# Kernel tuning notes

Hardware: AMD Instinct MI355X
Metric: run time of the kernel (lower is better)

## Reference

```python
import jax, jax.numpy as jnp
import numpy as np
import math

EMBED_SIZE = 2048
HEADS = 32
GROUPS = 8
HEAD_DIM = EMBED_SIZE // HEADS          # 64
HPG = HEADS // GROUPS                   # heads per group = 4
N, L = 4, 1024


def setup_inputs() -> dict:
    key = jax.random.key(0)
    k1, k2, k3, k4, k5 = jax.random.split(key, 5)
    values = jax.random.normal(k1, (N, L, EMBED_SIZE), dtype=jnp.float32)
    keys = jax.random.normal(k2, (N, L, EMBED_SIZE), dtype=jnp.float32)
    queries = jax.random.normal(k3, (N, L, EMBED_SIZE), dtype=jnp.float32)
    mask = jnp.ones((N, 1, 1, L, L), dtype=jnp.int32)
    # fc_out: Linear(heads*head_dim -> embed_size), torch default init ~ U(-1/sqrt(in), 1/sqrt(in))
    bound = 1.0 / math.sqrt(EMBED_SIZE)
    W_out = jax.random.uniform(k4, (EMBED_SIZE, EMBED_SIZE), jnp.float32, -bound, bound)
    b_out = jax.random.uniform(k5, (EMBED_SIZE,), jnp.float32, -bound, bound)
    return {"values": values, "keys": keys, "queries": queries, "mask": mask,
            "W_out": W_out, "b_out": b_out}


def reference(values, keys, queries, mask, W_out, b_out):
    n, q_len, _ = queries.shape
    k_len = keys.shape[1]
    # split into (N, L, groups, heads_per_group, head_dim)
    v = values.reshape(n, k_len, GROUPS, HPG, HEAD_DIM)
    k = keys.reshape(n, k_len, GROUPS, HPG, HEAD_DIM)
    q = queries.reshape(n, q_len, GROUPS, HPG, HEAD_DIM)
    # scores: (N, groups, heads_per_group, q, k)
    energy = jnp.einsum('nqghd,nkghd->nghqk', q, k)
    energy = jnp.where(mask == 0, jnp.float32(-1e20), energy)
    attn = jax.nn.softmax(energy / jnp.sqrt(jnp.float32(EMBED_SIZE)), axis=-1)
    out = jnp.einsum('nghqk,nkghd->nqghd', attn, v).reshape(n, q_len, EMBED_SIZE)
    return out @ W_out.T + b_out
```

## Files before the change

kernel.cpp:

```cpp
#include <hip/hip_runtime.h>
#include <math.h>


#define LSEQ 1024
#define EMB  2048

typedef __bf16 bf16x8 __attribute__((ext_vector_type(8)));
typedef __bf16 bf16x4 __attribute__((ext_vector_type(4)));
typedef float floatx4 __attribute__((ext_vector_type(4)));
typedef unsigned short ushort8v __attribute__((ext_vector_type(8)));

__device__ __forceinline__ float4 ld4(const float* p) { return *(const float4*)p; }

__device__ __forceinline__ unsigned short f2bf(float x) {
    unsigned u = __float_as_uint(x);
    u += 0x7FFFu + ((u >> 16) & 1u);
    return (unsigned short)(u >> 16);
}

__device__ __forceinline__ void gl_lds16(const void* g, void* l) {
    __builtin_amdgcn_global_load_lds((const __attribute__((address_space(1))) void*)g,
                                     (__attribute__((address_space(3))) void*)l, 16, 0, 0);
}

__device__ __forceinline__ void stage64w(const unsigned short* g, size_t gstride,
                                         unsigned short* lds, int t) {
    const int r  = t >> 3;
    const int sl = (t & 7) ^ (r & 7);
    gl_lds16(g + (size_t)r * gstride + sl * 8, lds + t * 8);
}

__device__ __forceinline__ void stage128(const unsigned short* g, size_t gstride,
                                         unsigned short* lds) {
    const int t = threadIdx.x;
    #pragma unroll
    for (int h = 0; h < 4; h++) {
        const int idx = h * 256 + t;
        const int r   = idx >> 3;
        const int sl  = (idx & 7) ^ (r & 7);
        gl_lds16(g + (size_t)r * gstride + sl * 8, lds + idx * 8);
    }
}

__device__ __forceinline__ bf16x8 frag_ld(const unsigned short* lds, int row, int seg) {
    return *(const bf16x8*)(lds + row * 64 + ((seg ^ (row & 7)) * 8));
}

__global__ __launch_bounds__(256)
void prep_all(const float* __restrict__ K, unsigned short* __restrict__ Kh,
              const float* __restrict__ W, unsigned short* __restrict__ Wh,
              const float* __restrict__ V, unsigned short* __restrict__ Vt) {
    __shared__ float tile[64][69];
    const int bid = blockIdx.x;
    const int t = threadIdx.x;
    if (bid < 4096) {
        const size_t i = ((size_t)bid * 256 + t) * 8;
        float4 a = ld4(K + i), b = ld4(K + i + 4);
        ushort8v h;
        h[0] = f2bf(a.x); h[1] = f2bf(a.y); h[2] = f2bf(a.z); h[3] = f2bf(a.w);
        h[4] = f2bf(b.x); h[5] = f2bf(b.y); h[6] = f2bf(b.z); h[7] = f2bf(b.w);
        *(ushort8v*)(Kh + i) = h;
    } else if (bid < 6144) {
        const size_t i = ((size_t)(bid - 4096) * 256 + t) * 8;
        float4 a = ld4(W + i), b = ld4(W + i + 4);
        ushort8v h;
        h[0] = f2bf(a.x); h[1] = f2bf(a.y); h[2] = f2bf(a.z); h[3] = f2bf(a.w);
        h[4] = f2bf(b.x); h[5] = f2bf(b.y); h[6] = f2bf(b.z); h[7] = f2bf(b.w);
        *(ushort8v*)(Wh + i) = h;
    } else {
        const int vb = bid - 6144;
        const int kc = vb & 15, h = (vb >> 4) & 31, n = vb >> 9;
        {
            const int rr = t >> 2, c4 = (t & 3) * 16;
            const float* src = V + ((size_t)(n * LSEQ + kc * 64 + rr)) * EMB + h * 64 + c4;
            #pragma unroll
            for (int j = 0; j < 4; j++)
                *(float4*)&tile[rr][c4 + j * 4] = ld4(src + j * 4);
        }
        __syncthreads();
        const int d = t >> 2, k16 = (t & 3) * 16;
        unsigned short* dst = Vt + ((size_t)((n * 32 + h) * 64 + d)) * 1024 + kc * 64 + k16;
        ushort8v o0, o1;
        #pragma unroll
        for (int j = 0; j < 8; j++) o0[j] = f2bf(tile[k16 + j][d]);
        #pragma unroll
        for (int j = 0; j < 8; j++) o1[j] = f2bf(tile[k16 + 8 + j][d]);
        *(ushort8v*)dst = o0;
        *(ushort8v*)(dst + 8) = o1;
    }
}

#define PSTR 76

#define ATTN_STEP(SK, SV)                                                                  \
    do {                                                                                   \
        floatx4 s[2][4];                                                                   \
        _Pragma("unroll")                                                                  \
        for (int set = 0; set < 2; set++)                                                  \
            _Pragma("unroll")                                                              \
            for (int kt = 0; kt < 4; kt++) s[set][kt] = (floatx4){0.f, 0.f, 0.f, 0.f};     \
        _Pragma("unroll")                                                                  \
        for (int kt = 0; kt < 4; kt++) {                                                   \
            _Pragma("unroll")                                                              \
            for (int hf = 0; hf < 2; hf++) {                                               \
                bf16x8 kf = frag_ld((SK), kt * 16 + lm, hf * 4 + cq);                      \
                s[0][kt] = __builtin_amdgcn_mfma_f32_16x16x32_bf16(kf, qf[0][hf],          \
                                                                   s[0][kt], 0, 0, 0);     \
                s[1][kt] = __builtin_amdgcn_mfma_f32_16x16x32_bf16(kf, qf[1][hf],          \
                                                                   s[1][kt], 0, 0, 0);     \
            }                                                                              \
        }                                                                                  \
        _Pragma("unroll")                                                                  \
        for (int set = 0; set < 2; set++) {                                                \
            _Pragma("unroll")                                                              \
            for (int kt = 0; kt < 4; kt++) {                                               \
                float p[4];                                                                \
                _Pragma("unroll")                                                          \
                for (int r = 0; r < 4; r++) {                                              \
                    p[r] = __builtin_amdgcn_exp2f(s[set][kt][r]);                          \
                    lpart[set] += p[r];                                                    \
                }                                                                          \
                bf16x4 pk;                                                                 \
                _Pragma("unroll")                                                          \
                for (int r = 0; r < 4; r++) pk[r] = (__bf16)p[r];                          \
                *(bf16x4*)(sP + (w32 + set * 16 + lm) * PSTR + kt * 16 + cq * 4) = pk;     \
            }                                                                              \
        }                                                                                  \
        _Pragma("unroll")                                                                  \
        for (int hf = 0; hf < 2; hf++) {                                                   \
            bf16x8 pf0 = *(const bf16x8*)(sP + (w32 + lm) * PSTR + hf * 32 + cq * 8);      \
            bf16x8 pf1 = *(const bf16x8*)(sP + (w32 + 16 + lm) * PSTR + hf * 32 + cq * 8); \
            _Pragma("unroll")                                                              \
            for (int dt = 0; dt < 4; dt++) {                                               \
                bf16x8 vf = frag_ld((SV), dt * 16 + lm, hf * 4 + cq);                      \
                o[0][dt] = __builtin_amdgcn_mfma_f32_16x16x32_bf16(pf0, vf,                \
                                                                   o[0][dt], 0, 0, 0);     \
                o[1][dt] = __builtin_amdgcn_mfma_f32_16x16x32_bf16(pf1, vf,                \
                                                                   o[1][dt], 0, 0, 0);     \
            }                                                                              \
        }                                                                                  \
    } while (0)

__global__ __launch_bounds__(512, 2)
void gqa_attn_mfma(const float* __restrict__ Qf, const unsigned short* __restrict__ Kh,
                   const unsigned short* __restrict__ Vt, unsigned short* __restrict__ Ah) {
    __shared__ unsigned short sA0[8192];
    __shared__ unsigned short sA1[8192];
    __shared__ unsigned short sP[256 * PSTR];

    const int bid  = blockIdx.x;
    const int hl   = bid & 127;
    const int qt   = bid >> 7;
    const int head = hl & 31;
    const int n    = hl >> 5;
    const int q0   = qt * 256;

    const int t = threadIdx.x, w = t >> 6, lane = t & 63;
    const int lm = lane & 15, cq = lane >> 4;
    const int w32 = w * 32;

    const float scale2 = 0.03187936190857805f;

    const unsigned short* Kb = Kh + ((size_t)(n * LSEQ)) * EMB + head * 64;
    const unsigned short* Vb = Vt + ((size_t)(n * 32 + head)) * 64 * 1024;

    stage64w(Kb, EMB, sA0, t);
    stage64w(Vb, 1024, sA0 + 4096, t);

    #pragma unroll
    for (int h = 0; h < 4; h++) {
        const int idx = h * 512 + t;
        const int r = idx >> 3;
        const int sl = idx & 7;
        const int sp = sl ^ (r & 7);
        const float* src = Qf + ((size_t)(n * LSEQ + q0 + r)) * EMB + head * 64 + sl * 8;
        float4 x0 = ld4(src), x1 = ld4(src + 4);
        float xs[8] = {x0.x, x0.y, x0.z, x0.w, x1.x, x1.y, x1.z, x1.w};
        ushort8v hv;
        #pragma unroll
        for (int j = 0; j < 8; j++) hv[j] = f2bf(xs[j] * scale2);
        *(ushort8v*)(sP + r * 64 + sp * 8) = hv;
    }
    __syncthreads();

    bf16x8 qf[2][2];
    #pragma unroll
    for (int set = 0; set < 2; set++)
        #pragma unroll
        for (int hf = 0; hf < 2; hf++)
            qf[set][hf] = frag_ld(sP, w32 + set * 16 + lm, hf * 4 + cq);
    __syncthreads();

    floatx4 o[2][4];
    #pragma unroll
    for (int set = 0; set < 2; set++)
        #pragma unroll
        for (int dt = 0; dt < 4; dt++) o[set][dt] = (floatx4){0.f, 0.f, 0.f, 0.f};
    float lpart[2] = {0.f, 0.f};

    for (int kb = 0; kb < 8; kb++) {
        const int kc0 = kb * 2;
        stage64w(Kb + (size_t)((kc0 + 1) * 64) * EMB, EMB, sA1, t);
        stage64w(Vb + (kc0 + 1) * 64, 1024, sA1 + 4096, t);
        ATTN_STEP(sA0, sA0 + 4096);
        __syncthreads();

        if (kb < 7) {
            stage64w(Kb + (size_t)((kc0 + 2) * 64) * EMB, EMB, sA0, t);
            stage64w(Vb + (kc0 + 2) * 64, 1024, sA0 + 4096, t);
        }
        ATTN_STEP(sA1, sA1 + 4096);
        __syncthreads();
    }

    #pragma unroll
    for (int set = 0; set < 2; set++) {
        float lred = lpart[set];
        lred += __shfl_xor(lred, 16);
        lred += __shfl_xor(lred, 32);
        const size_t obase =
            ((size_t)(n * LSEQ + q0 + w32 + set * 16 + cq * 4)) * EMB + head * 64 + lm;
        #pragma unroll
        for (int r = 0; r < 4; r++) {
            const float inv = 1.f / __shfl(lred, cq * 4 + r);
            #pragma unroll
            for (int dt = 0; dt < 4; dt++)
                Ah[obase + (size_t)r * EMB + dt * 16] = f2bf(o[set][dt][r] * inv);
        }
    }
}

#define OUT_STEP(SA, SB)                                                                   \
    do {                                                                                   \
        bf16x8 af[4][2], bf[4][2];                                                         \
        _Pragma("unroll")                                                                  \
        for (int i = 0; i < 4; i++)                                                        \
            _Pragma("unroll")                                                              \
            for (int kk = 0; kk < 2; kk++)                                                 \
                af[i][kk] = frag_ld((SA), wr * 64 + i * 16 + lm, kk * 4 + cq);             \
        _Pragma("unroll")                                                                  \
        for (int j = 0; j < 4; j++)                                                        \
            _Pragma("unroll")                                                              \
            for (int kk = 0; kk < 2; kk++)                                                 \
                bf[j][kk] = frag_ld((SB), wc * 64 + j * 16 + lm, kk * 4 + cq);             \
        _Pragma("unroll")                                                                  \
        for (int i = 0; i < 4; i++)                                                        \
            _Pragma("unroll")                                                              \
            for (int j = 0; j < 4; j++)                                                    \
                _Pragma("unroll")                                                          \
                for (int kk = 0; kk < 2; kk++)                                             \
                    acc[i][j] = __builtin_amdgcn_mfma_f32_16x16x32_bf16(af[i][kk],         \
                                                        bf[j][kk], acc[i][j], 0, 0, 0);    \
    } while (0)

__global__ __launch_bounds__(256, 2)
void out_proj_bf16(const unsigned short* __restrict__ A, const unsigned short* __restrict__ B,
                   const float* __restrict__ bias, float* __restrict__ C) {
    __shared__ unsigned short sA0[128 * 64];
    __shared__ unsigned short sB0[128 * 64];
    __shared__ unsigned short sA1[128 * 64];
    __shared__ unsigned short sB1[128 * 64];

    const int t = threadIdx.x, bid = blockIdx.x;
    const int nb = bid & 15, mb = bid >> 4;
    const int m0 = mb * 128, n0 = nb * 128;
    const int wave = t >> 6, lane = t & 63;
    const int wr = wave >> 1, wc = wave & 1;
    const int lm = lane & 15, cq = lane >> 4;

    floatx4 acc[4][4];
    #pragma unroll
    for (int i = 0; i < 4; i++)
        #pragma unroll
        for (int j = 0; j < 4; j++)
            acc[i][j] = (floatx4){0.f, 0.f, 0.f, 0.f};

    stage128(A + (size_t)m0 * 2048, 2048, sA0);
    stage128(B + (size_t)n0 * 2048, 2048, sB0);
    __syncthreads();

    for (int kb = 0; kb < 16; kb++) {
        const int kc0 = kb * 2;
        stage128(A + (size_t)m0 * 2048 + (kc0 + 1) * 64, 2048, sA1);
        stage128(B + (size_t)n0 * 2048 + (kc0 + 1) * 64, 2048, sB1);
        OUT_STEP(sA0, sB0);
        __syncthreads();

        if (kb < 15) {
            stage128(A + (size_t)m0 * 2048 + (kc0 + 2) * 64, 2048, sA0);
            stage128(B + (size_t)n0 * 2048 + (kc0 + 2) * 64, 2048, sB0);
        }
        OUT_STEP(sA1, sB1);
        __syncthreads();
    }

    const int lr = cq * 4;
    #pragma unroll
    for (int j = 0; j < 4; j++) {
        const int col = n0 + wc * 64 + j * 16 + lm;
        const float bv = bias[col];
        #pragma unroll
        for (int i = 0; i < 4; i++) {
            const int rowb = m0 + wr * 64 + i * 16 + lr;
            #pragma unroll
            for (int r = 0; r < 4; r++)
                C[(size_t)(rowb + r) * 2048 + col] = acc[i][j][r] + bv;
        }
    }
}

extern "C" void kernel_launch(void* const* d_in, const int* in_sizes, int n_in,
                              void* d_out, int out_size, void* d_ws, size_t ws_size,
                              hipStream_t stream) {
    const float* V = (const float*)d_in[0];
    const float* K = (const float*)d_in[1];
    const float* Q = (const float*)d_in[2];
    const float* W = (const float*)d_in[4];
    const float* b = (const float*)d_in[5];
    float* out = (float*)d_out;

    unsigned short* Ah = (unsigned short*)d_ws;
    unsigned short* Kh = Ah + (size_t)4096 * 2048;
    unsigned short* Vt = Kh + (size_t)4096 * 2048;
    unsigned short* Wh = Vt + (size_t)4 * 32 * 64 * 1024;

    prep_all<<<8192, 256, 0, stream>>>(K, Kh, W, Wh, V, Vt);
    gqa_attn_mfma<<<512, 512, 0, stream>>>(Q, Kh, Vt, Ah);
    out_proj_bf16<<<512, 256, 0, stream>>>(Ah, Wh, b, out);
}
```

Measured before the change: 242.3 us.

## Halve attention block to 128 queries and add MFMA wave priority hints

The attention kernel now uses 256-thread blocks covering 128 query rows instead of 512 threads over 256 rows, launching 1024 blocks. K/V staging is rewritten so each thread issues two 16-byte loads per tile. The Q staging buffer moves into the second K/V buffer, which shrinks LDS per block so three blocks can fit per CU. s_setprio raises wave priority around the MFMA sections. Each K/V tile is now fetched by twice as many blocks, adding global/L2 traffic, and fewer waves may be resident per CU.

```diff
diff --git a/kernel.cpp b/kernel.cpp
--- a/kernel.cpp
+++ b/kernel.cpp
@@ -23,11 +23,16 @@
                                      (__attribute__((address_space(3))) void*)l, 16, 0, 0);
 }
 
-__device__ __forceinline__ void stage64w(const unsigned short* g, size_t gstride,
-                                         unsigned short* lds, int t) {
-    const int r  = t >> 3;
-    const int sl = (t & 7) ^ (r & 7);
-    gl_lds16(g + (size_t)r * gstride + sl * 8, lds + t * 8);
+__device__ __forceinline__ void stage64(const unsigned short* g, size_t gstride,
+                                        unsigned short* lds) {
+    const int t = threadIdx.x;
+    #pragma unroll
+    for (int h = 0; h < 2; h++) {
+        const int idx = h * 256 + t;
+        const int r   = idx >> 3;
+        const int sl  = (idx & 7) ^ (r & 7);
+        gl_lds16(g + (size_t)r * gstride + sl * 8, lds + idx * 8);
+    }
 }
 
 __device__ __forceinline__ void stage128(const unsigned short* g, size_t gstride,
@@ -99,6 +104,7 @@
         for (int set = 0; set < 2; set++)                                                  \
             _Pragma("unroll")                                                              \
             for (int kt = 0; kt < 4; kt++) s[set][kt] = (floatx4){0.f, 0.f, 0.f, 0.f};     \
+        __builtin_amdgcn_s_setprio(1);                                                     \
         _Pragma("unroll")                                                                  \
         for (int kt = 0; kt < 4; kt++) {                                                   \
             _Pragma("unroll")                                                              \
@@ -110,6 +116,7 @@
                                                                    s[1][kt], 0, 0, 0);     \
             }                                                                              \
         }                                                                                  \
+        __builtin_amdgcn_s_setprio(0);                                                     \
         _Pragma("unroll")                                                                  \
         for (int set = 0; set < 2; set++) {                                                \
             _Pragma("unroll")                                                              \
@@ -126,6 +133,7 @@
                 *(bf16x4*)(sP + (w32 + set * 16 + lm) * PSTR + kt * 16 + cq * 4) = pk;     \
             }                                                                              \
         }                                                                                  \
+        __builtin_amdgcn_s_setprio(1);                                                     \
         _Pragma("unroll")                                                                  \
         for (int hf = 0; hf < 2; hf++) {                                                   \
             bf16x8 pf0 = *(const bf16x8*)(sP + (w32 + lm) * PSTR + hf * 32 + cq * 8);      \
@@ -139,21 +147,22 @@
                                                                    o[1][dt], 0, 0, 0);     \
             }                                                                              \
         }                                                                                  \
+        __builtin_amdgcn_s_setprio(0);                                                     \
     } while (0)
 
-__global__ __launch_bounds__(512, 2)
+__global__ __launch_bounds__(256, 3)
 void gqa_attn_mfma(const float* __restrict__ Qf, const unsigned short* __restrict__ Kh,
                    const unsigned short* __restrict__ Vt, unsigned short* __restrict__ Ah) {
     __shared__ unsigned short sA0[8192];
     __shared__ unsigned short sA1[8192];
-    __shared__ unsigned short sP[256 * PSTR];
+    __shared__ unsigned short sP[128 * PSTR];
 
     const int bid  = blockIdx.x;
     const int hl   = bid & 127;
     const int qt   = bid >> 7;
     const int head = hl & 31;
     const int n    = hl >> 5;
-    const int q0   = qt * 256;
+    const int q0   = qt * 128;
 
     const int t = threadIdx.x, w = t >> 6, lane = t & 63;
     const int lm = lane & 15, cq = lane >> 4;
@@ -164,12 +173,12 @@
     const unsigned short* Kb = Kh + ((size_t)(n * LSEQ)) * EMB + head * 64;
     const unsigned short* Vb = Vt + ((size_t)(n * 32 + head)) * 64 * 1024;
 
-    stage64w(Kb, EMB, sA0, t);
-    stage64w(Vb, 1024, sA0 + 4096, t);
+    stage64(Kb, EMB, sA0);
+    stage64(Vb, 1024, sA0 + 4096);
 
     #pragma unroll
     for (int h = 0; h < 4; h++) {
-        const int idx = h * 512 + t;
+        const int idx = h * 256 + t;
         const int r = idx >> 3;
         const int sl = idx & 7;
         const int sp = sl ^ (r & 7);
@@ -179,7 +188,7 @@
         ushort8v hv;
         #pragma unroll
         for (int j = 0; j < 8; j++) hv[j] = f2bf(xs[j] * scale2);
-        *(ushort8v*)(sP + r * 64 + sp * 8) = hv;
+        *(ushort8v*)(sA1 + r * 64 + sp * 8) = hv;
     }
     __syncthreads();
 
@@ -188,7 +197,7 @@
     for (int set = 0; set < 2; set++)
         #pragma unroll
         for (int hf = 0; hf < 2; hf++)
-            qf[set][hf] = frag_ld(sP, w32 + set * 16 + lm, hf * 4 + cq);
+            qf[set][hf] = frag_ld(sA1, w32 + set * 16 + lm, hf * 4 + cq);
     __syncthreads();
 
     floatx4 o[2][4];
@@ -200,14 +209,14 @@
 
     for (int kb = 0; kb < 8; kb++) {
         const int kc0 = kb * 2;
-        stage64w(Kb + (size_t)((kc0 + 1) * 64) * EMB, EMB, sA1, t);
-        stage64w(Vb + (kc0 + 1) * 64, 1024, sA1 + 4096, t);
+        stage64(Kb + (size_t)((kc0 + 1) * 64) * EMB, EMB, sA1);
+        stage64(Vb + (kc0 + 1) * 64, 1024, sA1 + 4096);
         ATTN_STEP(sA0, sA0 + 4096);
         __syncthreads();
 
         if (kb < 7) {
-            stage64w(Kb + (size_t)((kc0 + 2) * 64) * EMB, EMB, sA0, t);
-            stage64w(Vb + (kc0 + 2) * 64, 1024, sA0 + 4096, t);
+            stage64(Kb + (size_t)((kc0 + 2) * 64) * EMB, EMB, sA0);
+            stage64(Vb + (kc0 + 2) * 64, 1024, sA0 + 4096);
         }
         ATTN_STEP(sA1, sA1 + 4096);
         __syncthreads();
@@ -325,6 +334,6 @@
     unsigned short* Wh = Vt + (size_t)4 * 32 * 64 * 1024;
 
     prep_all<<<8192, 256, 0, stream>>>(K, Kh, W, Wh, V, Vt);
-    gqa_attn_mfma<<<512, 512, 0, stream>>>(Q, Kh, Vt, Ah);
+    gqa_attn_mfma<<<1024, 256, 0, stream>>>(Q, Kh, Vt, Ah);
     out_proj_bf16<<<512, 256, 0, stream>>>(Ah, Wh, b, out);
 }
```

Result: no change. 238.7 us (-1.5%).
